# Performance work log

Measured on AMD Instinct MI355X. Metric: run time of the kernel, lower is better.

The kernel has to match this reference:

```python
import jax, jax.numpy as jnp
import numpy as np

P = 16          # patch_size
EMBED = 768     # embed_dim
HEAD_DIM = 64   # embed_dim // num_heads
ROPE_BASE = 10000.0


def rope_2d(coords, head_dim, base):
    """Axial 2D RoPE. coords: (N, 2) int -> cos, sin each (N, head_dim).
    head_dim is split evenly over the two axes; within an axis, frequency
    pairs are repeated twice (standard rotate-pairs layout)."""
    dpa = head_dim // 2                                   # dims per axis
    inv_freq = 1.0 / (base ** (jnp.arange(0, dpa, 2, dtype=jnp.float32) / dpa))  # (dpa//2,)
    ang = coords.astype(jnp.float32)[:, :, None] * inv_freq[None, None, :]       # (N, 2, dpa//2)
    ang = jnp.repeat(ang, 2, axis=-1).reshape(coords.shape[0], head_dim)          # (N, head_dim)
    return jnp.cos(ang), jnp.sin(ang)


def setup_inputs() -> dict:
    key = jax.random.key(0)
    k1, k2 = jax.random.split(key, 2)
    B, C, H, W = 32, 3, 512, 512
    images = jax.random.normal(k1, (B, C, H, W), dtype=jnp.float32)
    patch_dim = C * P * P
    W_proj = jax.random.normal(k2, (patch_dim, EMBED), dtype=jnp.float32) * (patch_dim ** -0.5)
    b_proj = jnp.zeros((EMBED,), dtype=jnp.float32)
    return {"images": images, "W_proj": W_proj, "b_proj": b_proj}


def reference(images, W_proj, b_proj):
    B, C, H, W = images.shape
    Hp, Wp = H // P, W // P
    N = B * Hp * Wp
    # patchify: c (hp p1) (wp p2) -> (hp wp) (c p1 p2), packed across batch
    x = images.reshape(B, C, Hp, P, Wp, P).transpose(0, 2, 4, 1, 3, 5).reshape(N, C * P * P)
    tokens = x @ W_proj + b_proj                              # (N, EMBED)
    # per-image patch coordinates (identical grid for every image)
    ys, xs = jnp.meshgrid(jnp.arange(Hp), jnp.arange(Wp), indexing='ij')
    coords = jnp.stack([ys, xs], axis=-1).reshape(Hp * Wp, 2)
    patch_coords = jnp.tile(coords, (B, 1))                    # (N, 2)
    rope_cos, rope_sin = rope_2d(patch_coords, HEAD_DIM, ROPE_BASE)
    cu_seqlens = (jnp.arange(B + 1, dtype=jnp.int32) * (Hp * Wp))
    is_patch = jnp.ones((N,), dtype=bool)
    return tokens, cu_seqlens, patch_coords, rope_cos, rope_sin, is_patch
```

## Files before the change

kernel.cpp:

```cpp
#include <hip/hip_runtime.h>
#include <hip/hip_bf16.h>

typedef unsigned short u16;
typedef unsigned int   u32;
typedef __bf16 bf16x8 __attribute__((ext_vector_type(8)));
typedef float  f32x4  __attribute__((ext_vector_type(4)));

#define N_TOK 32768
constexpr long long OFF_TOKENS = 0;
constexpr long long OFF_CU     = 25165824LL;
constexpr long long OFF_COORDS = 25165857LL;
constexpr long long OFF_COS    = 25231393LL;
constexpr long long OFF_SIN    = 27328545LL;
constexpr long long OFF_ISP    = 29425697LL;

__device__ __forceinline__ void split_bf16(float v, u16& h, u16& l) {
    __hip_bfloat16 bh = __float2bfloat16(v);
    float fh = __bfloat162float(bh);
    __hip_bfloat16 bl = __float2bfloat16(v - fh);
    h = __builtin_bit_cast(u16, bh);
    l = __builtin_bit_cast(u16, bl);
}

__device__ __forceinline__ u32 pk2(float lo, float hi) {
    u32 a = (u32)__builtin_bit_cast(u16, __float2bfloat16(lo));
    u32 b = (u32)__builtin_bit_cast(u16, __float2bfloat16(hi));
    return a | (b << 16);
}

__global__ __launch_bounds__(128) void prep_w(const float* __restrict__ W,
                                              u16* __restrict__ wt) {
    const int n  = blockIdx.x;
    const int kg = threadIdx.x;
    if (kg >= 96) return;
    u16 h[8], l[8];
    #pragma unroll
    for (int r = 0; r < 8; r++)
        split_bf16(W[(size_t)(kg * 8 + r) * 768 + n], h[r], l[r]);
    uint4 H, L;
    H.x = (u32)h[0] | ((u32)h[1] << 16); H.y = (u32)h[2] | ((u32)h[3] << 16);
    H.z = (u32)h[4] | ((u32)h[5] << 16); H.w = (u32)h[6] | ((u32)h[7] << 16);
    L.x = (u32)l[0] | ((u32)l[1] << 16); L.y = (u32)l[2] | ((u32)l[3] << 16);
    L.z = (u32)l[4] | ((u32)l[5] << 16); L.w = (u32)l[6] | ((u32)l[7] << 16);
    *(uint4*)&wt[(size_t)n * 768 + kg * 8]          = H;
    *(uint4*)&wt[589824 + (size_t)n * 768 + kg * 8] = L;
}

__global__ __launch_bounds__(256) void patch_gemm_mfma(
    const float* __restrict__ img, const u16* __restrict__ wt,
    const float* __restrict__ bias, float* __restrict__ out)
{
    __shared__ __align__(16) char smem[24576];
    char* pAh = smem;
    char* pBh = smem + 8192;
    char* pBl = smem + 16384;

    const int tid = threadIdx.x;
    const int bn  = blockIdx.x;
    const int bm  = blockIdx.y;

    const int lane = tid & 63;
    const int wid  = tid >> 6;
    const int wm   = (wid >> 1) << 6;
    const int wn   = (wid & 1) << 6;
    const int lr   = lane & 15;
    const int lg   = lane >> 4;

    const int am  = tid & 127;
    const int alq = tid >> 7;
    const int m   = bm * 128 + am;
    const int bb  = m >> 10;
    const int hp  = (m & 1023) >> 5;
    const int wq  = m & 31;
    const float* abase = img + (size_t)bb * 786432 + (size_t)hp * 8192 + wq * 16;
    const int a_wb = am * 64 + ((alq ^ ((am >> 3) & 1)) << 5);

    const int bnl = tid >> 1;
    const int blq = tid & 1;
    const u16* wbh = wt + (size_t)(bn * 128 + bnl) * 768 + blq * 16;
    const u16* wbl = wbh + 589824;
    const int b_wb = bnl * 64 + ((blq ^ ((bnl >> 3) & 1)) << 5);

    const int swz  = (lr >> 3) & 1;
    const int a_rd = lr * 64 + (((lg >> 1) ^ swz) << 5) + ((lg & 1) << 4);

    f32x4 acc[4][4];
    #pragma unroll
    for (int i = 0; i < 4; i++)
        #pragma unroll
        for (int j = 0; j < 4; j++) acc[i][j] = {0.f, 0.f, 0.f, 0.f};

    float4 a0, a1, a2, a3;
    uint4 wh0, wh1, wl0, wl1;

#define LOAD_T(KT)                                                          \
    {   const float* ap = abase + ((KT) >> 3) * 262144 +                    \
                          (((KT) & 7) * 2 + alq) * 512;                     \
        a0 = *(const float4*)(ap);      a1 = *(const float4*)(ap + 4);      \
        a2 = *(const float4*)(ap + 8);  a3 = *(const float4*)(ap + 12);     \
        const u16* ph = wbh + (KT) * 32;                                    \
        wh0 = *(const uint4*)(ph);      wh1 = *(const uint4*)(ph + 8);      \
        const u16* pl = wbl + (KT) * 32;                                    \
        wl0 = *(const uint4*)(pl);      wl1 = *(const uint4*)(pl + 8); }

    LOAD_T(0);

    #pragma unroll 1
    for (int kt = 0; kt < 24; ++kt) {
        __syncthreads();

        uint4 H;
        H.x = pk2(a0.x, a0.y); H.y = pk2(a0.z, a0.w);
        H.z = pk2(a1.x, a1.y); H.w = pk2(a1.z, a1.w);
        *(uint4*)(pAh + a_wb) = H;
        H.x = pk2(a2.x, a2.y); H.y = pk2(a2.z, a2.w);
        H.z = pk2(a3.x, a3.y); H.w = pk2(a3.z, a3.w);
        *(uint4*)(pAh + a_wb + 16) = H;
        *(uint4*)(pBh + b_wb)      = wh0;
        *(uint4*)(pBh + b_wb + 16) = wh1;
        *(uint4*)(pBl + b_wb)      = wl0;
        *(uint4*)(pBl + b_wb + 16) = wl1;

        if (kt < 23) LOAD_T(kt + 1);

        __syncthreads();

        bf16x8 ah[4], bh4[4], bl4[4];
        #pragma unroll
        for (int i = 0; i < 4; i++)
            ah[i] = *(const bf16x8*)(pAh + (wm + i * 16) * 64 + a_rd);
        #pragma unroll
        for (int j = 0; j < 4; j++) {
            const int off = (wn + j * 16) * 64 + a_rd;
            bh4[j] = *(const bf16x8*)(pBh + off);
            bl4[j] = *(const bf16x8*)(pBl + off);
        }

        #pragma unroll
        for (int i = 0; i < 4; i++)
            #pragma unroll
            for (int j = 0; j < 4; j++) {
                acc[i][j] = __builtin_amdgcn_mfma_f32_16x16x32_bf16(ah[i], bh4[j], acc[i][j], 0, 0, 0);
                acc[i][j] = __builtin_amdgcn_mfma_f32_16x16x32_bf16(ah[i], bl4[j], acc[i][j], 0, 0, 0);
            }
    }
#undef LOAD_T

    float bv[4];
    #pragma unroll
    for (int j = 0; j < 4; j++) bv[j] = bias[bn * 128 + wn + j * 16 + lr];
    #pragma unroll
    for (int i = 0; i < 4; i++) {
        const int rb = bm * 128 + wm + i * 16 + lg * 4;
        #pragma unroll
        for (int j = 0; j < 4; j++) {
            const int cg = bn * 128 + wn + j * 16 + lr;
            #pragma unroll
            for (int r = 0; r < 4; r++)
                out[OFF_TOKENS + (size_t)(rb + r) * 768 + cg] = acc[i][j][r] + bv[j];
        }
    }
}

__global__ __launch_bounds__(256) void aux_kernel(float* __restrict__ out)
{
    const int idx = blockIdx.x * 256 + threadIdx.x;
    if (idx >= N_TOK * 32) return;
    const int n  = idx >> 5;
    const int jd = idx & 31;

    const int hp = (n & 1023) >> 5;
    const int wp = n & 31;

    const int coord = (jd < 16) ? hp : wp;
    const int j = jd & 15;
    const float freq = exp2f(-(float)j * 0.8304820237218406f);
    float s, c;
    sincosf((float)coord * freq, &s, &c);

    const long long off = (long long)n * 64 + jd * 2;
    *(float2*)(out + OFF_COS + off) = make_float2(c, c);
    *(float2*)(out + OFF_SIN + off) = make_float2(s, s);

    if (jd == 0) {
        out[OFF_COORDS + 2 * (long long)n]     = (float)hp;
        out[OFF_COORDS + 2 * (long long)n + 1] = (float)wp;
        out[OFF_ISP + n] = 1.0f;
    }
    if (jd == 1 && n < 33) {
        out[OFF_CU + n] = (float)(n * 1024);
    }
}

extern "C" void kernel_launch(void* const* d_in, const int* in_sizes, int n_in,
                              void* d_out, int out_size, void* d_ws, size_t ws_size,
                              hipStream_t stream) {
    const float* img  = (const float*)d_in[0];
    const float* W    = (const float*)d_in[1];
    const float* bias = (const float*)d_in[2];
    float* out = (float*)d_out;
    u16* wt = (u16*)d_ws;

    prep_w<<<768, 128, 0, stream>>>(W, wt);

    dim3 ggrid(6, 256);
    patch_gemm_mfma<<<ggrid, 256, 0, stream>>>(img, wt, bias, out);

    const int aux_elems = N_TOK * 32;
    aux_kernel<<<(aux_elems + 255) / 256, 256, 0, stream>>>(out);
}
```

Baseline: 289.8 us.

## Double-buffer GEMM tiles with direct global-to-LDS weight loads and 512-thread blocks

The weight prep kernel now writes pre-swizzled per-tile bf16 hi/lo blocks, so the GEMM can copy B tiles straight into LDS with global_load_lds instead of going through registers. The GEMM moves to 512 threads, 8 waves with 64x32 sub-tiles, and double-buffers the A and B LDS tiles so the next tile's loads overlap the current tile's MFMAs, using one barrier per step instead of two. Blocks are remapped with an XCD-aware swizzle of the linear block index to improve L2 locality. LDS use doubles to 48KB and the pipeline logic becomes more complex.

```diff
diff --git a/kernel.cpp b/kernel.cpp
--- a/kernel.cpp
+++ b/kernel.cpp
@@ -28,132 +28,145 @@
     return a | (b << 16);
 }
 
-__global__ __launch_bounds__(128) void prep_w(const float* __restrict__ W,
-                                              u16* __restrict__ wt) {
-    const int n  = blockIdx.x;
-    const int kg = threadIdx.x;
-    if (kg >= 96) return;
-    u16 h[8], l[8];
-    #pragma unroll
-    for (int r = 0; r < 8; r++)
-        split_bf16(W[(size_t)(kg * 8 + r) * 768 + n], h[r], l[r]);
-    uint4 H, L;
-    H.x = (u32)h[0] | ((u32)h[1] << 16); H.y = (u32)h[2] | ((u32)h[3] << 16);
-    H.z = (u32)h[4] | ((u32)h[5] << 16); H.w = (u32)h[6] | ((u32)h[7] << 16);
-    L.x = (u32)l[0] | ((u32)l[1] << 16); L.y = (u32)l[2] | ((u32)l[3] << 16);
-    L.z = (u32)l[4] | ((u32)l[5] << 16); L.w = (u32)l[6] | ((u32)l[7] << 16);
-    *(uint4*)&wt[(size_t)n * 768 + kg * 8]          = H;
-    *(uint4*)&wt[589824 + (size_t)n * 768 + kg * 8] = L;
-}
-
-__global__ __launch_bounds__(256) void patch_gemm_mfma(
-    const float* __restrict__ img, const u16* __restrict__ wt,
+__global__ __launch_bounds__(256) void prep_w(const float* __restrict__ W,
+                                              u16* __restrict__ wt2) {
+    const int bid = blockIdx.x;
+    const int bn  = bid / 24;
+    const int kt  = bid - bn * 24;
+    __shared__ u16 im[8192];
+    const int t  = threadIdx.x;
+    const int k  = t >> 3;
+    const int n0 = (t & 7) * 16;
+    const float* src = W + (size_t)(kt * 32 + k) * 768 + bn * 128 + n0;
+    #pragma unroll
+    for (int e = 0; e < 16; e++) {
+        const int n = n0 + e;
+        u16 h, l;
+        split_bf16(src[e], h, l);
+        const int p = (n * 64 + (((k >> 4) ^ ((n >> 3) & 1)) << 5) + (k & 15) * 2) >> 1;
+        im[p] = h;
+        im[4096 + p] = l;
+    }
+    __syncthreads();
+    uint4* g = (uint4*)(wt2 + (size_t)bid * 8192);
+    const uint4* s = (const uint4*)im;
+    #pragma unroll
+    for (int i = 0; i < 4; i++) g[t + i * 256] = s[t + i * 256];
+}
+
+__global__ __launch_bounds__(512, 4) void patch_gemm_mfma(
+    const float* __restrict__ img, const u16* __restrict__ wt2,
     const float* __restrict__ bias, float* __restrict__ out)
 {
-    __shared__ __align__(16) char smem[24576];
-    char* pAh = smem;
-    char* pBh = smem + 8192;
-    char* pBl = smem + 16384;
-
-    const int tid = threadIdx.x;
-    const int bn  = blockIdx.x;
-    const int bm  = blockIdx.y;
-
+    __shared__ __align__(16) char smem[49152];
+    char* pA0 = smem;
+    char* pA1 = smem + 8192;
+    char* pB0 = smem + 16384;
+    char* pB1 = smem + 32768;
+
+    const int L   = blockIdx.x;
+    const int c   = (L & 7) * 192 + (L >> 3);
+    const int bm  = c / 6;
+    const int bn  = c - bm * 6;
+    const int tb  = bn * 24;
+
+    const int tid  = threadIdx.x;
     const int lane = tid & 63;
     const int wid  = tid >> 6;
-    const int wm   = (wid >> 1) << 6;
-    const int wn   = (wid & 1) << 6;
+    const int wm   = (wid >> 2) << 6;
+    const int wn   = (wid & 3) << 5;
     const int lr   = lane & 15;
     const int lg   = lane >> 4;
 
-    const int am  = tid & 127;
-    const int alq = tid >> 7;
-    const int m   = bm * 128 + am;
-    const int bb  = m >> 10;
-    const int hp  = (m & 1023) >> 5;
-    const int wq  = m & 31;
+    const int am = tid & 127;
+    const int aq = tid >> 7;
+    const int m  = bm * 128 + am;
+    const int bb = m >> 10;
+    const int hp = (m & 1023) >> 5;
+    const int wq = m & 31;
     const float* abase = img + (size_t)bb * 786432 + (size_t)hp * 8192 + wq * 16;
-    const int a_wb = am * 64 + ((alq ^ ((am >> 3) & 1)) << 5);
-
-    const int bnl = tid >> 1;
-    const int blq = tid & 1;
-    const u16* wbh = wt + (size_t)(bn * 128 + bnl) * 768 + blq * 16;
-    const u16* wbl = wbh + 589824;
-    const int b_wb = bnl * 64 + ((blq ^ ((bnl >> 3) & 1)) << 5);
-
-    const int swz  = (lr >> 3) & 1;
-    const int a_rd = lr * 64 + (((lg >> 1) ^ swz) << 5) + ((lg & 1) << 4);
-
-    f32x4 acc[4][4];
+    const int a_wb = am * 64 + (((aq >> 1) ^ ((am >> 3) & 1)) << 5) + ((aq & 1) << 4);
+
+    const int a_rd = lr * 64 + (((lg >> 1) ^ ((lr >> 3) & 1)) << 5) + ((lg & 1) << 4);
+
+    f32x4 acc[4][2];
     #pragma unroll
     for (int i = 0; i < 4; i++)
         #pragma unroll
-        for (int j = 0; j < 4; j++) acc[i][j] = {0.f, 0.f, 0.f, 0.f};
-
-    float4 a0, a1, a2, a3;
-    uint4 wh0, wh1, wl0, wl1;
-
-#define LOAD_T(KT)                                                          \
-    {   const float* ap = abase + ((KT) >> 3) * 262144 +                    \
-                          (((KT) & 7) * 2 + alq) * 512;                     \
-        a0 = *(const float4*)(ap);      a1 = *(const float4*)(ap + 4);      \
-        a2 = *(const float4*)(ap + 8);  a3 = *(const float4*)(ap + 12);     \
-        const u16* ph = wbh + (KT) * 32;                                    \
-        wh0 = *(const uint4*)(ph);      wh1 = *(const uint4*)(ph + 8);      \
-        const u16* pl = wbl + (KT) * 32;                                    \
-        wl0 = *(const uint4*)(pl);      wl1 = *(const uint4*)(pl + 8); }
-
-    LOAD_T(0);
+        for (int j = 0; j < 2; j++) acc[i][j] = {0.f, 0.f, 0.f, 0.f};
+
+    float4 A0a, A0b, A1a, A1b;
+
+#define LOAD_A(ra, rb, T)                                                   \
+    {   const float* ap = abase + ((T) >> 3) * 262144 +                     \
+            (((T) & 7) * 2 + (aq >> 1)) * 512 + (aq & 1) * 8;               \
+        ra = *(const float4*)ap;  rb = *(const float4*)(ap + 4); }
+
+#define CVT_STORE(ra, rb, pdst)                                             \
+    {   uint4 Hq;                                                           \
+        Hq.x = pk2(ra.x, ra.y); Hq.y = pk2(ra.z, ra.w);                     \
+        Hq.z = pk2(rb.x, rb.y); Hq.w = pk2(rb.z, rb.w);                     \
+        *(uint4*)((pdst) + a_wb) = Hq; }
+
+#define GLOADB(T, dst)                                                      \
+    {   const char* s = (const char*)wt2 + (size_t)(tb + (T)) * 16384       \
+                        + (wid << 11) + (lane << 4);                        \
+        char* d = (dst) + (wid << 11);                                      \
+        __builtin_amdgcn_global_load_lds(                                   \
+            (const __attribute__((address_space(1))) u32*)s,                \
+            (__attribute__((address_space(3))) u32*)d, 16, 0, 0);           \
+        __builtin_amdgcn_global_load_lds(                                   \
+            (const __attribute__((address_space(1))) u32*)(s + 1024),       \
+            (__attribute__((address_space(3))) u32*)(d + 1024), 16, 0, 0); }
+
+#define COMPUTE(pAc, pBc)                                                   \
+    {   bf16x8 ahf[4], bhf[2], blf[2];                                      \
+        _Pragma("unroll")                                                   \
+        for (int i = 0; i < 4; i++)                                         \
+            ahf[i] = *(const bf16x8*)((pAc) + ((wm + i * 16) << 6) + a_rd); \
+        _Pragma("unroll")                                                   \
+        for (int j = 0; j < 2; j++) {                                       \
+            bhf[j] = *(const bf16x8*)((pBc) + ((wn + j * 16) << 6) + a_rd); \
+            blf[j] = *(const bf16x8*)((pBc) + 8192 + ((wn + j * 16) << 6) + a_rd); \
+        }                                                                   \
+        _Pragma("unroll")                                                   \
+        for (int i = 0; i < 4; i++)                                         \
+            _Pragma("unroll")                                               \
+            for (int j = 0; j < 2; j++) {                                   \
+                acc[i][j] = __builtin_amdgcn_mfma_f32_16x16x32_bf16(ahf[i], bhf[j], acc[i][j], 0, 0, 0); \
+                acc[i][j] = __builtin_amdgcn_mfma_f32_16x16x32_bf16(ahf[i], blf[j], acc[i][j], 0, 0, 0); \
+            } }
+
+    LOAD_A(A0a, A0b, 0);
+    GLOADB(0, pB0);
+    LOAD_A(A1a, A1b, 1);
+    CVT_STORE(A0a, A0b, pA0);
+    __syncthreads();
 
     #pragma unroll 1
-    for (int kt = 0; kt < 24; ++kt) {
+    for (int t = 0; t < 24; t += 2) {
+        if (t < 23) { CVT_STORE(A1a, A1b, pA1); GLOADB(t + 1, pB1); }
+        if (t < 22) LOAD_A(A0a, A0b, t + 2);
+        COMPUTE(pA0, pB0);
         __syncthreads();
-
-        uint4 H;
-        H.x = pk2(a0.x, a0.y); H.y = pk2(a0.z, a0.w);
-        H.z = pk2(a1.x, a1.y); H.w = pk2(a1.z, a1.w);
-        *(uint4*)(pAh + a_wb) = H;
-        H.x = pk2(a2.x, a2.y); H.y = pk2(a2.z, a2.w);
-        H.z = pk2(a3.x, a3.y); H.w = pk2(a3.z, a3.w);
-        *(uint4*)(pAh + a_wb + 16) = H;
-        *(uint4*)(pBh + b_wb)      = wh0;
-        *(uint4*)(pBh + b_wb + 16) = wh1;
-        *(uint4*)(pBl + b_wb)      = wl0;
-        *(uint4*)(pBl + b_wb + 16) = wl1;
-
-        if (kt < 23) LOAD_T(kt + 1);
-
+        if (t + 1 < 23) { CVT_STORE(A0a, A0b, pA0); GLOADB(t + 2, pB0); }
+        if (t + 1 < 22) LOAD_A(A1a, A1b, t + 3);
+        COMPUTE(pA1, pB1);
         __syncthreads();
-
-        bf16x8 ah[4], bh4[4], bl4[4];
-        #pragma unroll
-        for (int i = 0; i < 4; i++)
-            ah[i] = *(const bf16x8*)(pAh + (wm + i * 16) * 64 + a_rd);
-        #pragma unroll
-        for (int j = 0; j < 4; j++) {
-            const int off = (wn + j * 16) * 64 + a_rd;
-            bh4[j] = *(const bf16x8*)(pBh + off);
-            bl4[j] = *(const bf16x8*)(pBl + off);
-        }
-
-        #pragma unroll
-        for (int i = 0; i < 4; i++)
-            #pragma unroll
-            for (int j = 0; j < 4; j++) {
-                acc[i][j] = __builtin_amdgcn_mfma_f32_16x16x32_bf16(ah[i], bh4[j], acc[i][j], 0, 0, 0);
-                acc[i][j] = __builtin_amdgcn_mfma_f32_16x16x32_bf16(ah[i], bl4[j], acc[i][j], 0, 0, 0);
-            }
-    }
-#undef LOAD_T
-
-    float bv[4];
-    #pragma unroll
-    for (int j = 0; j < 4; j++) bv[j] = bias[bn * 128 + wn + j * 16 + lr];
+    }
+#undef LOAD_A
+#undef CVT_STORE
+#undef GLOADB
+#undef COMPUTE
+
+    float bv[2];
+    #pragma unroll
+    for (int j = 0; j < 2; j++) bv[j] = bias[bn * 128 + wn + j * 16 + lr];
     #pragma unroll
     for (int i = 0; i < 4; i++) {
         const int rb = bm * 128 + wm + i * 16 + lg * 4;
         #pragma unroll
-        for (int j = 0; j < 4; j++) {
+        for (int j = 0; j < 2; j++) {
             const int cg = bn * 128 + wn + j * 16 + lr;
             #pragma unroll
             for (int r = 0; r < 4; r++)
@@ -199,12 +212,11 @@
     const float* W    = (const float*)d_in[1];
     const float* bias = (const float*)d_in[2];
     float* out = (float*)d_out;
-    u16* wt = (u16*)d_ws;
-
-    prep_w<<<768, 128, 0, stream>>>(W, wt);
-
-    dim3 ggrid(6, 256);
-    patch_gemm_mfma<<<ggrid, 256, 0, stream>>>(img, wt, bias, out);
+    u16* wt2 = (u16*)d_ws;
+
+    prep_w<<<144, 256, 0, stream>>>(W, wt2);
+
+    patch_gemm_mfma<<<1536, 512, 0, stream>>>(img, wt2, bias, out);
 
     const int aux_elems = N_TOK * 32;
     aux_kernel<<<(aux_elems + 255) / 256, 256, 0, stream>>>(out);
```

Result: faster. 266.8 us (-7.9%).
